# Kernel tuning notes

Hardware: AMD Instinct MI355X
Metric: run time of the kernel (lower is better)

The kernel has to match this reference:

```python
import jax, jax.numpy as jnp
import numpy as np

B, S, HID, NH, KCLIP = 2, 1500, 1024, 16, 64
HD = HID // NH  # 64


def setup_inputs() -> dict:
    key = jax.random.key(0)
    ks = jax.random.split(key, 16)
    std = 0.02
    inp = {
        "query": jax.random.normal(ks[0], (B, S, HID), jnp.float32),
        "key": jax.random.normal(ks[1], (B, S, HID), jnp.float32),
        "value": jax.random.normal(ks[2], (B, S, HID), jnp.float32),
        # per-head projection weights, stacked over heads: [NH, HID, HD]
        "Wq": jax.random.normal(ks[3], (NH, HID, HD), jnp.float32) * std,
        "bq": jax.random.normal(ks[4], (NH, HD), jnp.float32) * std,
        "Wk": jax.random.normal(ks[5], (NH, HID, HD), jnp.float32) * std,
        "bk": jax.random.normal(ks[6], (NH, HD), jnp.float32) * std,
        "Wv": jax.random.normal(ks[7], (NH, HID, HD), jnp.float32) * std,
        "bv": jax.random.normal(ks[8], (NH, HD), jnp.float32) * std,
        # Shaw relative-position embedding tables: [2k+1, HD]
        "pe_k": jax.random.normal(ks[9], (2 * KCLIP + 1, HD), jnp.float32) * std,
        "pe_v": jax.random.normal(ks[10], (2 * KCLIP + 1, HD), jnp.float32) * std,
        # output projection (torch Linear stored as x @ W + b here)
        "W_fc": jax.random.normal(ks[11], (HID, HID), jnp.float32) * std,
        "b_fc": jax.random.normal(ks[12], (HID,), jnp.float32) * std,
    }
    return inp


def _rel_bias(pe, length, k_clip):
    idx = jnp.arange(length)
    dist = jnp.clip(idx[None, :] - idx[:, None], -k_clip, k_clip) + k_clip
    return pe[dist]  # [S, S, HD]


def reference(query, key, value, Wq, bq, Wk, bk, Wv, bv, pe_k, pe_v, W_fc, b_fc):
    head_dim = Wq.shape[-1]
    seq = query.shape[1]
    k_clip = (pe_k.shape[0] - 1) // 2

    kb = _rel_bias(pe_k, seq, k_clip)  # [S, S, HD]
    vb = _rel_bias(pe_v, seq, k_clip)  # [S, S, HD]

    # batched per-head projections: [B, NH, S, HD]
    Q = jnp.einsum('bsh,nhd->bnsd', query, Wq) + bq[None, :, None, :]
    K = jnp.einsum('bsh,nhd->bnsd', key, Wk) + bk[None, :, None, :]
    V = jnp.einsum('bsh,nhd->bnsd', value, Wv) + bv[None, :, None, :]

    # content term + Shaw relative-key bias term
    scores = jnp.einsum('bnqd,bnkd->bnqk', Q, K) \
           + jnp.einsum('bnqd,qkd->bnqk', Q, kb)
    scores = scores / jnp.sqrt(jnp.asarray(head_dim, scores.dtype))

    w = jax.nn.softmax(scores, axis=-1)  # [B, NH, S, S]

    out = jnp.einsum('bnqk,bnkd->bnqd', w, V) \
        + jnp.einsum('bnqk,qkd->bnqd', w, vb)

    # concat heads (head order matches ModuleList concatenation)
    hidden = out.transpose(0, 2, 1, 3).reshape(query.shape[0], seq, -1)
    return hidden @ W_fc + b_fc
```

## Files before the change

### kernel.cpp

```cpp
#include <hip/hip_runtime.h>
#include <math.h>

#define B_     2
#define S_     1500
#define HID_   1024
#define NH_    16
#define HD_    64
#define M_     (B_*S_)
#define SP_    1536
#define LOG2E  1.4426950408889634f

typedef short bf16x8 __attribute__((ext_vector_type(8)));
typedef short bf16x4 __attribute__((ext_vector_type(4)));
typedef float f32x4  __attribute__((ext_vector_type(4)));

__device__ __forceinline__ float b2f(short s) {
    unsigned u = ((unsigned)(unsigned short)s) << 16;
    return __uint_as_float(u);
}
__device__ __forceinline__ short f2b(float f) {
    unsigned u = __float_as_uint(f);
    unsigned r = (u + 0x7FFFu + ((u >> 16) & 1u)) >> 16;
    return (short)r;
}
__device__ __forceinline__ void gload16(const short* src, short* lds) {
    __builtin_amdgcn_global_load_lds(
        (const __attribute__((address_space(1))) void*)src,
        (__attribute__((address_space(3))) void*)lds, 16, 0, 0);
}

__global__ __launch_bounds__(256) void cvt_act3(
    const float* __restrict__ q, const float* __restrict__ k,
    const float* __restrict__ v, short* __restrict__ oq,
    short* __restrict__ ok, short* __restrict__ ov)
{
    const float* src = blockIdx.y == 0 ? q : blockIdx.y == 1 ? k : v;
    short* dst       = blockIdx.y == 0 ? oq : blockIdx.y == 1 ? ok : ov;
    int i = blockIdx.x * 256 + threadIdx.x;
    const float4* p = (const float4*)(src + (size_t)i * 8);
    float4 a = p[0], b = p[1];
    bf16x8 o;
    o[0]=f2b(a.x); o[1]=f2b(a.y); o[2]=f2b(a.z); o[3]=f2b(a.w);
    o[4]=f2b(b.x); o[5]=f2b(b.y); o[6]=f2b(b.z); o[7]=f2b(b.w);
    *(bf16x8*)(dst + (size_t)i * 8) = o;
}

__global__ __launch_bounds__(256) void prep_w(
    const float* __restrict__ Wq, const float* __restrict__ Wk,
    const float* __restrict__ Wv, const float* __restrict__ Wfc,
    const float* __restrict__ pe_k, const float* __restrict__ pe_v,
    short* __restrict__ Wqt, short* __restrict__ Wkt, short* __restrict__ Wvt,
    short* __restrict__ Wfh, short* __restrict__ Wfl,
    short* __restrict__ pe_kb, short* __restrict__ pe_vt)
{
    int z = blockIdx.x, tid = threadIdx.x;
    if (z == 1024) {
        for (int s = tid; s < 144 * 64; s += 256) {
            int j = s >> 6, d = s & 63;
            pe_kb[s] = (j < 129) ? f2b(pe_k[j * 64 + d]) : (short)0;
        }
        for (int s = tid; s < 64 * 160; s += 256) {
            int d = s / 160, j = s - d * 160;
            pe_vt[s] = (j < 129) ? f2b(pe_v[j * 64 + d]) : (short)0;
        }
        return;
    }
    __shared__ float T[64][65];
    const float* src; short* dhi; short* dlo = nullptr;
    int C, c0, r0; float scale = 1.f;
    if (z < 768) {
        int widx = z >> 8, rem = z & 255;
        int h = rem >> 4, rt = rem & 15;
        src = (widx == 0 ? Wq : widx == 1 ? Wk : Wv) + (size_t)h * 1024 * 64;
        dhi = (widx == 0 ? Wqt : widx == 1 ? Wkt : Wvt) + (size_t)h * 64 * 1024;
        scale = (widx == 0) ? 0.125f * LOG2E : 1.0f;
        C = 64; c0 = 0; r0 = rt * 64;
    } else {
        int idx = z - 768;
        src = Wfc; dhi = Wfh; dlo = Wfl;
        C = 1024; c0 = (idx >> 4) * 64; r0 = (idx & 15) * 64;
    }
#pragma unroll
    for (int i = 0; i < 4; ++i) {
        int slot = tid + i * 256;
        int r = slot >> 4, cg = (slot & 15) * 4;
        float4 v = *(const float4*)(src + (size_t)(r0 + r) * C + c0 + cg);
        T[r][cg+0] = v.x*scale; T[r][cg+1] = v.y*scale;
        T[r][cg+2] = v.z*scale; T[r][cg+3] = v.w*scale;
    }
    __syncthreads();
#pragma unroll
    for (int i = 0; i < 16; ++i) {
        int slot = tid + i * 256;
        int c = slot >> 6, r = slot & 63;
        float v = T[r][c];
        short hi = f2b(v);
        size_t o = (size_t)(c0 + c) * 1024 + r0 + r;
        dhi[o] = hi;
        if (dlo) dlo[o] = f2b(v - b2f(hi));
    }
}

__device__ __forceinline__ void gemm_core(
    const short* __restrict__ Ahi, const short* __restrict__ Alo,
    const short* __restrict__ Bhi, const short* __restrict__ Blo,
    int kIters, int m0, int n0, short* As, short* Bs, f32x4 (&acc)[4][4])
{
    const int tid = threadIdx.x, w = tid >> 6, lane = tid & 63;
    const int l15 = lane & 15, lr4 = lane >> 4;
    const int wr = w >> 1, wc = w & 1;

    for (int it = 0; it < kIters; ++it) {
        int kt = it * 64;
        int seg = kt >> 10, kk0 = kt & 1023;
        const short* Aseg = (seg == 1) ? Alo : Ahi;
        const short* Bseg = (seg == 2) ? Blo : Bhi;
        __syncthreads();
#pragma unroll
        for (int c = 0; c < 4; ++c) {
            int slot = (w * 4 + c) * 64 + lane;
            int r = slot >> 3, cb = slot & 7;
            int sm = m0 + r; sm = sm < M_ ? sm : M_ - 1;
            gload16(Aseg + (size_t)sm * 1024 + kk0 + ((cb ^ (r & 7)) * 8),
                    As + (size_t)(w * 4 + c) * 512);
            gload16(Bseg + (size_t)(n0 + r) * 1024 + kk0 + ((cb ^ (r & 7)) * 8),
                    Bs + (size_t)(w * 4 + c) * 512);
        }
        __syncthreads();
#pragma unroll
        for (int kh = 0; kh < 2; ++kh) {
            bf16x8 aF[4], bF[4];
#pragma unroll
            for (int mi = 0; mi < 4; ++mi) {
                int r = wr * 64 + mi * 16 + l15;
                aF[mi] = *(const bf16x8*)(As + r * 64 + (((kh*4+lr4) ^ (r & 7)) * 8));
            }
#pragma unroll
            for (int ni = 0; ni < 4; ++ni) {
                int r = wc * 64 + ni * 16 + l15;
                bF[ni] = *(const bf16x8*)(Bs + r * 64 + (((kh*4+lr4) ^ (r & 7)) * 8));
            }
#pragma unroll
            for (int mi = 0; mi < 4; ++mi)
#pragma unroll
                for (int ni = 0; ni < 4; ++ni)
                    acc[mi][ni] = __builtin_amdgcn_mfma_f32_16x16x32_bf16(
                        aF[mi], bF[ni], acc[mi][ni], 0, 0, 0);
        }
    }
}

__global__ __launch_bounds__(256) void gemm_qkv(
    const short* __restrict__ qb, const short* __restrict__ kb,
    const short* __restrict__ vb, const short* __restrict__ Wqt,
    const short* __restrict__ Wkt, const short* __restrict__ Wvt,
    const float* __restrict__ bq, const float* __restrict__ bk,
    const float* __restrict__ bv,
    short* __restrict__ Qp, short* __restrict__ Kp, short* __restrict__ Vp)
{
    __shared__ short As[128 * 64];
    __shared__ short Bs[128 * 64];
    const int z = blockIdx.z;
    const short* A  = z == 0 ? qb : z == 1 ? kb : vb;
    const short* Bw = z == 0 ? Wqt : z == 1 ? Wkt : Wvt;
    const float* bias = z == 0 ? bq : z == 1 ? bk : bv;
    const float bscale = z == 0 ? 0.125f * LOG2E : 1.0f;
    short* out = z == 0 ? Qp : z == 1 ? Kp : Vp;
    const int m0 = blockIdx.x * 128, n0 = blockIdx.y * 128;

    f32x4 zf = {0.f,0.f,0.f,0.f};
    f32x4 acc[4][4];
#pragma unroll
    for (int i = 0; i < 4; ++i)
#pragma unroll
        for (int j = 0; j < 4; ++j) acc[i][j] = zf;

    gemm_core(A, A, Bw, Bw, 16, m0, n0, As, Bs, acc);

    const int tid = threadIdx.x, w = tid >> 6, lane = tid & 63;
    const int l15 = lane & 15, lr4 = lane >> 4;
    const int wr = w >> 1, wc = w & 1;
#pragma unroll
    for (int mi = 0; mi < 4; ++mi)
#pragma unroll
        for (int rr = 0; rr < 4; ++rr) {
            int m = m0 + wr * 64 + mi * 16 + lr4 * 4 + rr;
            if (m >= M_) continue;
            int b = m / S_, s = m - b * S_;
#pragma unroll
            for (int ni = 0; ni < 4; ++ni) {
                int n = n0 + wc * 64 + ni * 16 + l15;
                float v = acc[mi][ni][rr] + bias[n] * bscale;
                int h = n >> 6, d = n & 63;
                out[(((size_t)(b * NH_ + h)) * S_ + s) * HD_ + d] = f2b(v);
            }
        }
}

__global__ __launch_bounds__(256) void gemm_fc(
    const short* __restrict__ Ahi, const short* __restrict__ Alo,
    const short* __restrict__ Bhi, const short* __restrict__ Blo,
    const float* __restrict__ bias, float* __restrict__ out)
{
    __shared__ short As[128 * 64];
    __shared__ short Bs[128 * 64];
    const int m0 = blockIdx.x * 128, n0 = blockIdx.y * 128;
    f32x4 zf = {0.f,0.f,0.f,0.f};
    f32x4 acc[4][4];
#pragma unroll
    for (int i = 0; i < 4; ++i)
#pragma unroll
        for (int j = 0; j < 4; ++j) acc[i][j] = zf;

    gemm_core(Ahi, Alo, Bhi, Blo, 32, m0, n0, As, Bs, acc);

    const int tid = threadIdx.x, w = tid >> 6, lane = tid & 63;
    const int l15 = lane & 15, lr4 = lane >> 4;
    const int wr = w >> 1, wc = w & 1;
#pragma unroll
    for (int mi = 0; mi < 4; ++mi)
#pragma unroll
        for (int rr = 0; rr < 4; ++rr) {
            int m = m0 + wr * 64 + mi * 16 + lr4 * 4 + rr;
            if (m >= M_) continue;
#pragma unroll
            for (int ni = 0; ni < 4; ++ni) {
                int n = n0 + wc * 64 + ni * 16 + l15;
                out[(size_t)m * 1024 + n] = acc[mi][ni][rr] + bias[n];
            }
        }
}

__global__ __launch_bounds__(256) void vtrans(
    const short* __restrict__ Vp, short* __restrict__ Vtg)
{
    __shared__ short T[64][72];
    const int bh = blockIdx.y, s0 = blockIdx.x * 64, tid = threadIdx.x;
    const size_t kv = (size_t)bh * S_ * 64;
#pragma unroll
    for (int i = 0; i < 2; ++i) {
        int slot = tid + i * 256;
        int r = slot >> 3, cb = slot & 7;
        int ss = s0 + r; ss = ss < S_ ? ss : S_ - 1;
        bf16x8 v = *(const bf16x8*)(Vp + kv + (size_t)ss * 64 + cb * 8);
        *(bf16x8*)(&T[r][cb * 8]) = v;
    }
    __syncthreads();
#pragma unroll
    for (int i = 0; i < 2; ++i) {
        int slot = tid + i * 256;
        int d = slot >> 3, cg = slot & 7;
        bf16x8 v;
#pragma unroll
        for (int j = 0; j < 8; ++j) {
            int kk = 32 * (cg >> 2) + ((j >> 2) & 1) * 16 + (cg & 3) * 4 + (j & 3);
            v[j] = T[kk][d];
        }
        *(bf16x8*)(Vtg + ((size_t)bh * 64 + d) * SP_ + s0 + cg * 8) = v;
    }
}

__global__ __launch_bounds__(256) void attn_mfma(
    const short* __restrict__ Qb, const short* __restrict__ Kb,
    const short* __restrict__ Vtg, const short* __restrict__ pe_kb,
    const short* __restrict__ pe_vt,
    short* __restrict__ hid_hi, short* __restrict__ hid_lo)
{
    __shared__ short Kc[128 * 64];
    __shared__ short Vt[64 * 128];
    __shared__ short qpe[64 * 144];
    __shared__ short wsm[64 * 160];

    const int tid = threadIdx.x, w = tid >> 6, lane = tid & 63;
    const int l15 = lane & 15, lr4 = lane >> 4;
    const int lg = (blockIdx.x & 7) * 96 + (blockIdx.x >> 3);
    const int bh = lg / 24, bx = lg - bh * 24;
    const int q0 = bx * 64;
    const int qw = q0 + w * 16;
    const int myq = qw + l15;
    const int myrow = w * 16 + l15;
    const size_t kv  = (size_t)bh * S_ * HD_;
    const size_t vtb = (size_t)bh * 64 * SP_;

    {
        short ini = f2b(-1e30f);
        bf16x8 iv;
#pragma unroll
        for (int i = 0; i < 8; ++i) iv[i] = ini;
        short* base = wsm + w * 16 * 160;
#pragma unroll
        for (int i = 0; i < 5; ++i)
            *(bf16x8*)(base + (size_t)(i * 64 + lane) * 8) = iv;
    }
#pragma unroll
    for (int cc = 0; cc < 2; ++cc) {
        int slot = (w * 2 + cc) * 64 + lane;
        int r = slot >> 3, cb = slot & 7;
        int sq = q0 + r; sq = sq < S_ ? sq : S_ - 1;
        gload16(Qb + kv + (size_t)sq * 64 + ((cb ^ (r & 7)) * 8),
                Kc + (size_t)(w * 2 + cc) * 512);
    }
    __syncthreads();

    bf16x8 qA[2];
    {
        int r = myrow;
        qA[0] = *(const bf16x8*)(Kc + r * 64 + ((lr4 ^ (r & 7)) * 8));
        qA[1] = *(const bf16x8*)(Kc + r * 64 + (((4 + lr4) ^ (r & 7)) * 8));
    }

    f32x4 zf = {0.f,0.f,0.f,0.f};
#pragma unroll
    for (int jt = 0; jt < 9; ++jt) {
        f32x4 a = zf;
#pragma unroll
        for (int kh = 0; kh < 2; ++kh) {
            bf16x8 pf = *(const bf16x8*)(pe_kb + (size_t)(jt * 16 + l15) * 64 + kh * 32 + lr4 * 8);
            a = __builtin_amdgcn_mfma_f32_16x16x32_bf16(pf, qA[kh], a, 0, 0, 0);
        }
        bf16x4 pk;
#pragma unroll
        for (int rr = 0; rr < 4; ++rr) pk[rr] = f2b(a[rr]);
        *(bf16x4*)(qpe + (size_t)myrow * 144 + jt * 16 + lr4 * 4) = pk;
    }
    const float qpe0   = b2f(qpe[myrow * 144 + 0]);
    const float qpe128 = b2f(qpe[myrow * 144 + 128]);
    __syncthreads();

    float m = 0.f, s0s = 0.f, s1s = 0.f;
    f32x4 o[4];
#pragma unroll
    for (int t = 0; t < 4; ++t) o[t] = zf;

    for (int c = 0; c < 12; ++c) {
        const int kc = c * 128;
#pragma unroll
        for (int cc = 0; cc < 4; ++cc) {
            int slot = (w * 4 + cc) * 64 + lane;
            int rK = slot >> 3, cbK = slot & 7;
            int sk = kc + rK; sk = sk < S_ ? sk : S_ - 1;
            gload16(Kb + kv + (size_t)sk * 64 + ((cbK ^ (rK & 7)) * 8),
                    Kc + (size_t)(w * 4 + cc) * 512);
            int rV = slot >> 4, cbV = slot & 15;
            gload16(Vtg + vtb + (size_t)rV * SP_ + kc + ((cbV ^ (rV & 7)) * 8),
                    Vt + (size_t)(w * 4 + cc) * 512);
        }
        __syncthreads();

        const bool lo0 = (kc +  63 - qw) <= -64, hi0 = (kc       - (qw + 15)) >= 64;
        const bool lo1 = (kc + 127 - qw) <= -64, hi1 = (kc + 64  - (qw + 15)) >= 64;
        const bool mx0 = !(lo0 || hi0), mx1 = !(lo1 || hi1);
        const float ub0 = lo0 ? qpe0 : qpe128;
        const float ub1 = lo1 ? qpe0 : qpe128;

        float rm = -1e30f;
        bf16x8 pa[2][2];
#pragma unroll
        for (int t8 = 0; t8 < 8; ++t8) {
            f32x4 s = zf;
#pragma unroll
            for (int kh = 0; kh < 2; ++kh) {
                int r = t8 * 16 + l15;
                bf16x8 kB = *(const bf16x8*)(Kc + r * 64 + (((kh*4+lr4) ^ (r & 7)) * 8));
                s = __builtin_amdgcn_mfma_f32_16x16x32_bf16(kB, qA[kh], s, 0, 0, 0);
            }
            const int h = t8 >> 2, tt = t8 & 3;
            const int wn = tt >> 1, sl = (tt & 1) * 4;
            const bool mx = h ? mx1 : mx0;
            const bool alo = h ? lo1 : lo0;
            const float ub = h ? ub1 : ub0;
#pragma unroll
            for (int rr = 0; rr < 4; ++rr) {
                int k = kc + t8 * 16 + lr4 * 4 + rr;
                int rel = k - myq;
                float v;
                if (mx) {
                    int jc = rel < -64 ? 0 : (rel > 64 ? 128 : rel + 64);
                    v = s[rr] + b2f(qpe[myrow * 144 + jc]);
                } else {
                    v = s[rr] + ub;
                }
                if (k >= S_) v = -1e30f;
                rm = fmaxf(rm, v);
                if (mx && rel > -64 && rel < 64)
                    wsm[myrow * 160 + rel + 64] = f2b(v);
                float p2 = exp2f(v - m);
                pa[h][wn][sl + rr] = f2b(p2);
                if (mx) {
                    if (rel <= -64) s0s += p2; else if (rel >= 64) s1s += p2;
                } else if (alo) s0s += p2; else s1s += p2;
            }
        }

        __builtin_amdgcn_s_setprio(1);
#pragma unroll
        for (int h = 0; h < 2; ++h)
#pragma unroll
            for (int wn = 0; wn < 2; ++wn)
#pragma unroll
                for (int td = 0; td < 4; ++td) {
                    int r = td * 16 + l15;
                    int cbv = h * 8 + wn * 4 + lr4;
                    bf16x8 vB = *(const bf16x8*)(Vt + r * 128 + ((cbv ^ (r & 7)) * 8));
                    o[td] = __builtin_amdgcn_mfma_f32_16x16x32_bf16(pa[h][wn], vB, o[td], 0, 0, 0);
                }
        __builtin_amdgcn_s_setprio(0);

        rm = fmaxf(rm, __shfl_xor(rm, 16));
        rm = fmaxf(rm, __shfl_xor(rm, 32));
        if (!__all(rm <= m + 8.f)) {
            float nm = fmaxf(m, rm);
            float fac = exp2f(m - nm);
            m = nm; s0s *= fac; s1s *= fac;
            float fo[4];
#pragma unroll
            for (int rr = 0; rr < 4; ++rr) fo[rr] = __shfl(fac, lr4 * 4 + rr);
#pragma unroll
            for (int t = 0; t < 4; ++t)
#pragma unroll
                for (int rr = 0; rr < 4; ++rr) o[t][rr] *= fo[rr];
        }

        __syncthreads();
    }

    s0s += __shfl_xor(s0s, 16); s0s += __shfl_xor(s0s, 32);
    s1s += __shfl_xor(s1s, 16); s1s += __shfl_xor(s1s, 32);

    short* rowp = wsm + (size_t)myrow * 160;
    float midsum = 0.f;
#pragma unroll
    for (int cc = 0; cc < 5; ++cc) {
        int off = (cc * 4 + lr4) * 8;
        bf16x8 mv = *(const bf16x8*)(rowp + off);
        bf16x8 ev;
#pragma unroll
        for (int jj = 0; jj < 8; ++jj) {
            float e = exp2f(b2f(mv[jj]) - m);
            ev[jj] = f2b(e);
            midsum += e;
        }
        *(bf16x8*)(rowp + off) = ev;
    }
    midsum += __shfl_xor(midsum, 16); midsum += __shfl_xor(midsum, 32);
    const float linv = 1.f / (s0s + s1s + midsum);
    if (lr4 == 0) { rowp[0] = f2b(s0s); rowp[128] = f2b(s1s); }

#pragma unroll
    for (int jh = 0; jh < 5; ++jh) {
        bf16x8 aW = *(const bf16x8*)(wsm + (size_t)myrow * 160 + jh * 32 + lr4 * 8);
#pragma unroll
        for (int td = 0; td < 4; ++td) {
            bf16x8 bW = *(const bf16x8*)(pe_vt + (size_t)(td * 16 + l15) * 160 + jh * 32 + lr4 * 8);
            o[td] = __builtin_amdgcn_mfma_f32_16x16x32_bf16(aW, bW, o[td], 0, 0, 0);
        }
    }

    {
        float fo[4];
#pragma unroll
        for (int rr = 0; rr < 4; ++rr) fo[rr] = __shfl(linv, lr4 * 4 + rr);
#pragma unroll
        for (int td = 0; td < 4; ++td)
#pragma unroll
            for (int rr = 0; rr < 4; ++rr) o[td][rr] *= fo[rr];
    }

#pragma unroll
    for (int td = 0; td < 4; ++td)
#pragma unroll
        for (int rr = 0; rr < 4; ++rr) {
            int qrow = lr4 * 4 + rr;
            int d = td * 16 + l15;
            int inner = (((d >> 2) ^ ((qrow & 7) << 1)) << 2) + (d & 3);
            float v = o[td][rr];
            short hi = f2b(v);
            wsm[(w * 16 + qrow) * 160 + inner] = hi;
            qpe[(w * 16 + qrow) * 144 + inner] = f2b(v - b2f(hi));
        }
    {
        int b = bh >> 4, h = bh & 15;
        int qrow = lane >> 2;
        int q = q0 + w * 16 + qrow;
#pragma unroll
        for (int i = 0; i < 2; ++i) {
            int cb = (lane & 3) * 2 + i;
            int qws = (cb * 2) ^ ((qrow & 7) << 1);
            bf16x8 hv = *(const bf16x8*)(wsm + (w * 16 + qrow) * 160 + qws * 4);
            bf16x8 lv = *(const bf16x8*)(qpe + (w * 16 + qrow) * 144 + qws * 4);
            if (q < S_) {
                size_t oo = ((size_t)(b * S_ + q)) * 1024 + h * 64 + cb * 8;
                *(bf16x8*)(hid_hi + oo) = hv;
                *(bf16x8*)(hid_lo + oo) = lv;
            }
        }
    }
}

extern "C" void kernel_launch(void* const* d_in, const int* in_sizes, int n_in,
                              void* d_out, int out_size, void* d_ws, size_t ws_size,
                              hipStream_t stream)
{
    const float* query = (const float*)d_in[0];
    const float* key   = (const float*)d_in[1];
    const float* value = (const float*)d_in[2];
    const float* Wq    = (const float*)d_in[3];
    const float* bq    = (const float*)d_in[4];
    const float* Wk    = (const float*)d_in[5];
    const float* bk    = (const float*)d_in[6];
    const float* Wv    = (const float*)d_in[7];
    const float* bv    = (const float*)d_in[8];
    const float* pe_k  = (const float*)d_in[9];
    const float* pe_v  = (const float*)d_in[10];
    const float* W_fc  = (const float*)d_in[11];
    const float* b_fc  = (const float*)d_in[12];

    char* W = (char*)d_ws;
    short* qb   = (short*)(W + 0);
    short* kb   = (short*)(W + 6291456);
    short* vb   = (short*)(W + 12582912);
    short* Vtg  = vb;
    short* Wqt  = (short*)(W + 18874368);
    short* Wkt  = (short*)(W + 20971520);
    short* Wvt  = (short*)(W + 23068672);
    short* Wfh  = (short*)(W + 25165824);
    short* Wfl  = (short*)(W + 27262976);
    short* Qp   = (short*)(W + 29360128);
    short* Kp   = (short*)(W + 35651584);
    short* Vp   = (short*)(W + 41943040);
    short* pekb = (short*)(W + 48234496);
    short* pevt = (short*)(W + 48252928);
    short* hidh = qb;
    short* hidl = kb;

    cvt_act3<<<dim3(1500, 3), 256, 0, stream>>>(query, key, value, qb, kb, vb);
    prep_w<<<1025, 256, 0, stream>>>(Wq, Wk, Wv, W_fc, pe_k, pe_v,
                                     Wqt, Wkt, Wvt, Wfh, Wfl, pekb, pevt);
    gemm_qkv<<<dim3(24, 8, 3), 256, 0, stream>>>(qb, kb, vb, Wqt, Wkt, Wvt,
                                                 bq, bk, bv, Qp, Kp, Vp);
    vtrans<<<dim3(24, 32), 256, 0, stream>>>(Vp, Vtg);
    attn_mfma<<<768, 256, 0, stream>>>(Qp, Kp, Vtg, pekb, pevt, hidh, hidl);
    gemm_fc<<<dim3(24, 8), 256, 0, stream>>>(hidh, hidl, Wfh, Wfl, b_fc, (float*)d_out);
}
```

Baseline: 262.7 us.

## Load Q/K/V MFMA operands directly from global memory instead of LDS staging

Removes the shared-memory staging buffers for Q, K and the transposed V in the attention kernel, so each wave reads its MFMA operands straight from global memory (relying on L1/L2 caching), and drops the per-chunk __syncthreads barriers. With less LDS per block, launch bounds now request 4 blocks per CU to raise occupancy. The cost is that the four waves of a block each fetch the same K/V tiles redundantly from cache, with uncoalesced 16-byte per-lane accesses and no explicit prefetch overlap.

```diff
diff --git a/kernel.cpp b/kernel.cpp
--- a/kernel.cpp
+++ b/kernel.cpp
@@ -260,14 +260,12 @@
     }
 }
 
-__global__ __launch_bounds__(256) void attn_mfma(
+__global__ __launch_bounds__(256, 4) void attn_mfma(
     const short* __restrict__ Qb, const short* __restrict__ Kb,
     const short* __restrict__ Vtg, const short* __restrict__ pe_kb,
     const short* __restrict__ pe_vt,
     short* __restrict__ hid_hi, short* __restrict__ hid_lo)
 {
-    __shared__ short Kc[128 * 64];
-    __shared__ short Vt[64 * 128];
     __shared__ short qpe[64 * 144];
     __shared__ short wsm[64 * 160];
 
@@ -292,21 +290,13 @@
         for (int i = 0; i < 5; ++i)
             *(bf16x8*)(base + (size_t)(i * 64 + lane) * 8) = iv;
     }
-#pragma unroll
-    for (int cc = 0; cc < 2; ++cc) {
-        int slot = (w * 2 + cc) * 64 + lane;
-        int r = slot >> 3, cb = slot & 7;
-        int sq = q0 + r; sq = sq < S_ ? sq : S_ - 1;
-        gload16(Qb + kv + (size_t)sq * 64 + ((cb ^ (r & 7)) * 8),
-                Kc + (size_t)(w * 2 + cc) * 512);
-    }
-    __syncthreads();
 
     bf16x8 qA[2];
     {
-        int r = myrow;
-        qA[0] = *(const bf16x8*)(Kc + r * 64 + ((lr4 ^ (r & 7)) * 8));
-        qA[1] = *(const bf16x8*)(Kc + r * 64 + (((4 + lr4) ^ (r & 7)) * 8));
+        int sq = myq < S_ ? myq : S_ - 1;
+        const short* qp = Qb + kv + (size_t)sq * 64 + lr4 * 8;
+        qA[0] = *(const bf16x8*)(qp);
+        qA[1] = *(const bf16x8*)(qp + 32);
     }
 
     f32x4 zf = {0.f,0.f,0.f,0.f};
@@ -325,7 +315,6 @@
     }
     const float qpe0   = b2f(qpe[myrow * 144 + 0]);
     const float qpe128 = b2f(qpe[myrow * 144 + 128]);
-    __syncthreads();
 
     float m = 0.f, s0s = 0.f, s1s = 0.f;
     f32x4 o[4];
@@ -334,18 +323,6 @@
 
     for (int c = 0; c < 12; ++c) {
         const int kc = c * 128;
-#pragma unroll
-        for (int cc = 0; cc < 4; ++cc) {
-            int slot = (w * 4 + cc) * 64 + lane;
-            int rK = slot >> 3, cbK = slot & 7;
-            int sk = kc + rK; sk = sk < S_ ? sk : S_ - 1;
-            gload16(Kb + kv + (size_t)sk * 64 + ((cbK ^ (rK & 7)) * 8),
-                    Kc + (size_t)(w * 4 + cc) * 512);
-            int rV = slot >> 4, cbV = slot & 15;
-            gload16(Vtg + vtb + (size_t)rV * SP_ + kc + ((cbV ^ (rV & 7)) * 8),
-                    Vt + (size_t)(w * 4 + cc) * 512);
-        }
-        __syncthreads();
 
         const bool lo0 = (kc +  63 - qw) <= -64, hi0 = (kc       - (qw + 15)) >= 64;
         const bool lo1 = (kc + 127 - qw) <= -64, hi1 = (kc + 64  - (qw + 15)) >= 64;
@@ -357,13 +334,13 @@
         bf16x8 pa[2][2];
 #pragma unroll
         for (int t8 = 0; t8 < 8; ++t8) {
-            f32x4 s = zf;
-#pragma unroll
-            for (int kh = 0; kh < 2; ++kh) {
-                int r = t8 * 16 + l15;
-                bf16x8 kB = *(const bf16x8*)(Kc + r * 64 + (((kh*4+lr4) ^ (r & 7)) * 8));
-                s = __builtin_amdgcn_mfma_f32_16x16x32_bf16(kB, qA[kh], s, 0, 0, 0);
-            }
+            int sk = kc + t8 * 16 + l15; sk = sk < S_ ? sk : S_ - 1;
+            const short* kp = Kb + kv + (size_t)sk * 64 + lr4 * 8;
+            bf16x8 k0 = *(const bf16x8*)(kp);
+            bf16x8 k1 = *(const bf16x8*)(kp + 32);
+            f32x4 s = __builtin_amdgcn_mfma_f32_16x16x32_bf16(k0, qA[0], zf, 0, 0, 0);
+            s = __builtin_amdgcn_mfma_f32_16x16x32_bf16(k1, qA[1], s, 0, 0, 0);
+
             const int h = t8 >> 2, tt = t8 & 3;
             const int wn = tt >> 1, sl = (tt & 1) * 4;
             const bool mx = h ? mx1 : mx0;
@@ -401,7 +378,7 @@
                 for (int td = 0; td < 4; ++td) {
                     int r = td * 16 + l15;
                     int cbv = h * 8 + wn * 4 + lr4;
-                    bf16x8 vB = *(const bf16x8*)(Vt + r * 128 + ((cbv ^ (r & 7)) * 8));
+                    bf16x8 vB = *(const bf16x8*)(Vtg + vtb + (size_t)r * SP_ + kc + cbv * 8);
                     o[td] = __builtin_amdgcn_mfma_f32_16x16x32_bf16(pa[h][wn], vB, o[td], 0, 0, 0);
                 }
         __builtin_amdgcn_s_setprio(0);
@@ -420,8 +397,6 @@
 #pragma unroll
                 for (int rr = 0; rr < 4; ++rr) o[t][rr] *= fo[rr];
         }
-
-        __syncthreads();
     }
 
     s0s += __shfl_xor(s0s, 16); s0s += __shfl_xor(s0s, 32);
```

After: 267.0 us. Within noise of the previous version (+1.6%).
